# Kernel optimization log

Measured on AMD Instinct MI355X. Metric: run time of the kernel, lower is better.

## Reference

```python
import jax, jax.numpy as jnp
import numpy as np

TEMP = 0.05
EPS = 1e-12


def setup_inputs() -> dict:
    key = jax.random.key(0)
    k1, k2, k3, k4 = jax.random.split(key, 4)
    B, D, N = 2048, 128, 100000
    inputs = jax.random.normal(k1, (B, D), dtype=jnp.float32)
    indexes = jax.random.randint(k2, (B,), 0, N, dtype=jnp.int64)
    labels = jax.random.randint(k3, (N,), 0, N, dtype=jnp.int64)
    feats = jax.random.normal(k4, (N, D), dtype=jnp.float32)
    # memory bank rows are kept L2-normalized by the module's update logic
    features = feats / jnp.linalg.norm(feats, axis=1, keepdims=True)
    return {"inputs": inputs, "indexes": indexes, "labels": labels, "features": features}


def reference(inputs, indexes, labels, features):
    # F.normalize(inputs, dim=1)
    inputs_n = inputs / jnp.maximum(jnp.linalg.norm(inputs, axis=1, keepdims=True), EPS)
    # targets = labels[indexes]
    targets = labels[indexes]
    # logits = inputs_n @ features.T / temp  -> [B, N]
    logits = jnp.matmul(inputs_n, features.T) / TEMP
    # cross-entropy with mean reduction
    logz = jax.nn.logsumexp(logits, axis=1)
    picked = jnp.take_along_axis(logits, targets[:, None], axis=1)[:, 0]
    loss = jnp.mean(logz - picked)
    return loss
```

## Files before the change

### kernel.cpp

```cpp
#include <hip/hip_runtime.h>

typedef float f32x4 __attribute__((ext_vector_type(4)));
typedef int   int4v __attribute__((ext_vector_type(4)));
typedef int   int8v __attribute__((ext_vector_type(8)));

#define AS1 __attribute__((address_space(1)))
#define AS3 __attribute__((address_space(3)))

#define NROWS 2048
#define NCOLS 100000
#define NPAD  100352
#define NCHUNK 98
#define K2C  28.853900817779268f
#define PADC 7.2552607e-7f
#define SCLA 0x7F7F7F7Fu
#define SCLB 0x7C7C7C7Cu

__global__ void k_prep(const float* __restrict__ X, const int* __restrict__ idx,
                       const int* __restrict__ lab, const float* __restrict__ F,
                       unsigned short* __restrict__ A8, float* __restrict__ picked) {
  int wid = threadIdx.x >> 6, lane = threadIdx.x & 63;
  int row = blockIdx.x * 4 + wid;
  int t = lab[idx[row]];
  float2 v = ((const float2*)(X + (size_t)row * 128))[lane];
  float2 f = ((const float2*)(F + (size_t)t * 128))[lane];
  float ss = v.x * v.x + v.y * v.y;
  float dp = v.x * f.x + v.y * f.y;
#pragma unroll
  for (int m = 1; m < 64; m <<= 1) {
    ss += __shfl_xor(ss, m, 64);
    dp += __shfl_xor(dp, m, 64);
  }
  float invn = 1.0f / fmaxf(sqrtf(ss), 1e-12f);
  float s = invn * K2C;
  int w = __builtin_amdgcn_cvt_pk_fp8_f32(v.x * s, v.y * s, 0, false);
  A8[row * 64 + lane] = (unsigned short)(w & 0xFFFF);
  if (lane == 0) picked[row] = 20.0f * dp * invn;
}

__global__ void k_conv(const float* __restrict__ F, unsigned char* __restrict__ Fq) {
  const int NG8 = NPAD * 16;
  const int NV8 = NCOLS * 16;
  int stride = gridDim.x * blockDim.x;
  for (int g = blockIdx.x * blockDim.x + threadIdx.x; g < NG8; g += stride) {
    float4 a = make_float4(0.f, 0.f, 0.f, 0.f), b = a;
    if (g < NV8) {
      a = ((const float4*)F)[2 * g];
      b = ((const float4*)F)[2 * g + 1];
    }
    int w0 = __builtin_amdgcn_cvt_pk_fp8_f32(a.x * 8.f, a.y * 8.f, 0, false);
    w0 = __builtin_amdgcn_cvt_pk_fp8_f32(a.z * 8.f, a.w * 8.f, w0, true);
    int w1 = __builtin_amdgcn_cvt_pk_fp8_f32(b.x * 8.f, b.y * 8.f, 0, false);
    w1 = __builtin_amdgcn_cvt_pk_fp8_f32(b.z * 8.f, b.w * 8.f, w1, true);
    ((int2*)Fq)[g] = make_int2(w0, w1);
  }
}

__global__ __launch_bounds__(256, 2) void k_gemm(
    const unsigned short* __restrict__ A8,
    const unsigned char* __restrict__ Fq,
    float* __restrict__ part) {
  __shared__ unsigned char ring[3][64 * 128];
  __shared__ float xpose[4][64];
  const int tid = threadIdx.x;
  const int wid = tid >> 6, lane = tid & 63;
  const int lrow = lane & 15, lk = lane >> 4;

  const int slot = blockIdx.x >> 3;
  const int xcd  = blockIdx.x & 7;
  const int mtile = slot & 7;
  const int chunk = (slot >> 3) * 8 + xcd;
  if (chunk >= NCHUNK) return;
  const int row0 = mtile * 256 + wid * 64;

  const unsigned char* A8b = (const unsigned char*)A8;
  int8v af[4];
#pragma unroll
  for (int mf = 0; mf < 4; ++mf) {
    const unsigned char* ap = A8b + (size_t)(row0 + mf * 16 + lrow) * 128 + lk * 32;
    ((int4v*)&af[mf])[0] = *(const int4v*)ap;
    ((int4v*)&af[mf])[1] = *(const int4v*)(ap + 16);
  }

  float racc[4][4];
#pragma unroll
  for (int mf = 0; mf < 4; ++mf)
#pragma unroll
    for (int j = 0; j < 4; ++j) racc[mf][j] = 0.f;

  f32x4 cinit = (f32x4){-K2C, -K2C, -K2C, -K2C};

  const int nbase = chunk * 1024;

  auto issue1 = [&](unsigned char* dst, int h, int it) {
    int off16 = it * 256 + tid;
    int col = off16 >> 3, up = off16 & 7;
    int ul = up ^ (col & 7);
    const unsigned char* src = Fq + (size_t)(nbase + h * 64 + col) * 128 + ul * 16;
    __builtin_amdgcn_global_load_lds((const AS1 void*)src,
                                     (AS3 void*)(dst + off16 * 16), 16, 0, 0);
  };

  auto half_body = [&](const unsigned char* sb, unsigned char* stDst, int hst) {
#pragma unroll
    for (int j = 0; j < 4; ++j) {
      int c = j * 16 + lrow;
      const unsigned char* cb = sb + c * 128;
      int x = c & 7;
      int8v b8;
      ((int4v*)&b8)[0] = *(const int4v*)(cb + (((lk * 2)     ^ x) * 16));
      ((int4v*)&b8)[1] = *(const int4v*)(cb + (((lk * 2 + 1) ^ x) * 16));
      if (stDst && (j & 1) == 0) issue1(stDst, hst, j >> 1);
      f32x4 acc[4];
#pragma unroll
      for (int mf = 0; mf < 4; ++mf)
        acc[mf] = __builtin_amdgcn_mfma_scale_f32_16x16x128_f8f6f4(
            af[mf], b8, cinit, 0, 0, 0, SCLA, 0, SCLB);
#pragma unroll
      for (int mf = 0; mf < 4; ++mf)
#pragma unroll
        for (int jj = 0; jj < 4; ++jj)
          racc[mf][jj] += __builtin_amdgcn_exp2f(acc[mf][jj]);
    }
  };

#pragma unroll
  for (int h = 0; h < 2; ++h)
#pragma unroll
    for (int it = 0; it < 2; ++it) issue1(&ring[h][0], h, it);

  int rs = 0;
#pragma unroll 1
  for (int h = 0; h < 14; ++h) {
    asm volatile("s_waitcnt vmcnt(2)" ::: "memory");
    __builtin_amdgcn_s_barrier();
    int ss = rs + 2 - (rs >= 1 ? 3 : 0);
    half_body(&ring[rs][0], &ring[ss][0], h + 2);
    rs = (rs == 2) ? 0 : rs + 1;
  }
  asm volatile("s_waitcnt vmcnt(2)" ::: "memory");
  __builtin_amdgcn_s_barrier();
  half_body(&ring[rs][0], nullptr, 0);
  rs = (rs == 2) ? 0 : rs + 1;
  asm volatile("s_waitcnt vmcnt(0)" ::: "memory");
  __builtin_amdgcn_s_barrier();
  half_body(&ring[rs][0], nullptr, 0);

#pragma unroll
  for (int mf = 0; mf < 4; ++mf)
#pragma unroll
    for (int j = 0; j < 4; ++j) {
      float v = racc[mf][j];
      v += __shfl_xor(v, 1, 64);
      v += __shfl_xor(v, 2, 64);
      v += __shfl_xor(v, 4, 64);
      v += __shfl_xor(v, 8, 64);
      if (lrow == 0) xpose[wid][mf * 16 + lk * 4 + j] = v;
    }
  __syncthreads();
  part[(size_t)chunk * NROWS + row0 + lane] = xpose[wid][lane];
}

__global__ void k_loss1(const float* __restrict__ part, float* __restrict__ psum) {
  int rb = blockIdx.x & 7, cb = blockIdx.x >> 3;
  int b = rb * 256 + threadIdx.x;
  float s = 0.f;
#pragma unroll
  for (int k = 0; k < 14; ++k)
    s += part[(size_t)(cb * 14 + k) * NROWS + b];
  psum[(size_t)cb * NROWS + b] = s;
}

__global__ void k_final(const float* __restrict__ psum, const float* __restrict__ picked,
                        float* __restrict__ out) {
  int tid = threadIdx.x;
  float lb = 0.f;
#pragma unroll
  for (int rr = 0; rr < 2; ++rr) {
    int b = rr * 1024 + tid;
    float tot = 0.f;
#pragma unroll
    for (int cb = 0; cb < 7; ++cb) tot += psum[(size_t)cb * NROWS + b];
    tot -= PADC;
    lb += 20.0f + logf(tot) - picked[b];
  }
#pragma unroll
  for (int m = 1; m < 64; m <<= 1) lb += __shfl_xor(lb, m, 64);
  __shared__ float red[16];
  if ((tid & 63) == 0) red[tid >> 6] = lb;
  __syncthreads();
  if (tid == 0) {
    float s = 0.f;
#pragma unroll
    for (int i = 0; i < 16; ++i) s += red[i];
    out[0] = s * (1.0f / 2048.0f);
  }
}

extern "C" void kernel_launch(void* const* d_in, const int* in_sizes, int n_in,
                              void* d_out, int out_size, void* d_ws, size_t ws_size,
                              hipStream_t stream) {
  const float* inputs  = (const float*)d_in[0];
  const int*   indexes = (const int*)d_in[1];
  const int*   labels  = (const int*)d_in[2];
  const float* feats   = (const float*)d_in[3];
  float* out = (float*)d_out;

  char* ws = (char*)d_ws;
  unsigned short* A8 = (unsigned short*)(ws + 0);
  unsigned char*  Fq = (unsigned char*)(ws + 262144);
  float* part   = (float*)(ws + 13107200);
  float* psum   = (float*)(ws + 13910016);
  float* picked = (float*)(ws + 13967360);

  hipLaunchKernelGGL(k_prep,  dim3(512),  dim3(256),  0, stream, inputs, indexes, labels, feats, A8, picked);
  hipLaunchKernelGGL(k_conv,  dim3(2048), dim3(256),  0, stream, feats, Fq);
  hipLaunchKernelGGL(k_gemm,  dim3(832),  dim3(256),  0, stream, A8, Fq, part);
  hipLaunchKernelGGL(k_loss1, dim3(56),   dim3(256),  0, stream, part, psum);
  hipLaunchKernelGGL(k_final, dim3(1),    dim3(1024), 0, stream, psum, picked, out);
}
```

Measured before the change: 67.29 us.

## Give each wave a private double-buffered B tile to remove block barriers

Each of the four waves now stages its own copy of the 64-column feature tile into a private double-buffered LDS region and waits only on its own vmcnt/lgkmcnt, so the per-step block-wide barriers are gone. The intent is to let waves run out of lockstep and remove barrier stalls. In exchange, global and L2 load traffic for B goes up fourfold, since every wave loads the whole tile instead of a quarter. LDS use grows from 24 KB to 64 KB per block, which may limit occupancy under launch_bounds(256,2).

```diff
diff --git a/kernel.cpp b/kernel.cpp
--- a/kernel.cpp
+++ b/kernel.cpp
@@ -60,7 +60,7 @@
     const unsigned short* __restrict__ A8,
     const unsigned char* __restrict__ Fq,
     float* __restrict__ part) {
-  __shared__ unsigned char ring[3][64 * 128];
+  __shared__ unsigned char ring[4][2][64 * 128];
   __shared__ float xpose[4][64];
   const int tid = threadIdx.x;
   const int wid = tid >> 6, lane = tid & 63;
@@ -92,16 +92,21 @@
 
   const int nbase = chunk * 1024;
 
-  auto issue1 = [&](unsigned char* dst, int h, int it) {
-    int off16 = it * 256 + tid;
-    int col = off16 >> 3, up = off16 & 7;
-    int ul = up ^ (col & 7);
-    const unsigned char* src = Fq + (size_t)(nbase + h * 64 + col) * 128 + ul * 16;
-    __builtin_amdgcn_global_load_lds((const AS1 void*)src,
-                                     (AS3 void*)(dst + off16 * 16), 16, 0, 0);
+  auto stageHalf = [&](int sl, int h) {
+    unsigned char* dst = &ring[wid][sl][0];
+#pragma unroll
+    for (int it = 0; it < 8; ++it) {
+      int u = it * 64 + lane;
+      int col = u >> 3, up = u & 7;
+      int ul = up ^ (col & 7);
+      const unsigned char* src = Fq + (size_t)(nbase + h * 64 + col) * 128 + ul * 16;
+      __builtin_amdgcn_global_load_lds((const AS1 void*)src,
+                                       (AS3 void*)(dst + u * 16), 16, 0, 0);
+    }
   };
 
-  auto half_body = [&](const unsigned char* sb, unsigned char* stDst, int hst) {
+  auto half_compute = [&](int sl) {
+    const unsigned char* sb = &ring[wid][sl][0];
 #pragma unroll
     for (int j = 0; j < 4; ++j) {
       int c = j * 16 + lrow;
@@ -110,7 +115,6 @@
       int8v b8;
       ((int4v*)&b8)[0] = *(const int4v*)(cb + (((lk * 2)     ^ x) * 16));
       ((int4v*)&b8)[1] = *(const int4v*)(cb + (((lk * 2 + 1) ^ x) * 16));
-      if (stDst && (j & 1) == 0) issue1(stDst, hst, j >> 1);
       f32x4 acc[4];
 #pragma unroll
       for (int mf = 0; mf < 4; ++mf)
@@ -124,27 +128,20 @@
     }
   };
 
-#pragma unroll
-  for (int h = 0; h < 2; ++h)
-#pragma unroll
-    for (int it = 0; it < 2; ++it) issue1(&ring[h][0], h, it);
-
-  int rs = 0;
+  stageHalf(0, 0);
+  stageHalf(1, 1);
+
 #pragma unroll 1
   for (int h = 0; h < 14; ++h) {
-    asm volatile("s_waitcnt vmcnt(2)" ::: "memory");
-    __builtin_amdgcn_s_barrier();
-    int ss = rs + 2 - (rs >= 1 ? 3 : 0);
-    half_body(&ring[rs][0], &ring[ss][0], h + 2);
-    rs = (rs == 2) ? 0 : rs + 1;
-  }
-  asm volatile("s_waitcnt vmcnt(2)" ::: "memory");
-  __builtin_amdgcn_s_barrier();
-  half_body(&ring[rs][0], nullptr, 0);
-  rs = (rs == 2) ? 0 : rs + 1;
+    asm volatile("s_waitcnt vmcnt(8)" ::: "memory");
+    half_compute(h & 1);
+    asm volatile("s_waitcnt lgkmcnt(0)" ::: "memory");
+    stageHalf(h & 1, h + 2);
+  }
+  asm volatile("s_waitcnt vmcnt(8)" ::: "memory");
+  half_compute(0);
   asm volatile("s_waitcnt vmcnt(0)" ::: "memory");
-  __builtin_amdgcn_s_barrier();
-  half_body(&ring[rs][0], nullptr, 0);
+  half_compute(1);
 
 #pragma unroll
   for (int mf = 0; mf < 4; ++mf)
```

After: 68.18 us. About the same (+1.3%).
